# Performance work log

Hardware: AMD Instinct MI355X
Metric: run time of the kernel (lower is better)

## Reference

```python
import jax, jax.numpy as jnp
import numpy as np

B, T, D = 32, 2048, 1024
H = D  # dim_h = dim_k in build()


def setup_inputs() -> dict:
    key = jax.random.key(0)
    ks = jax.random.split(key, 8)
    t = jax.random.normal(ks[0], (B, T, D), dtype=jnp.float32)
    a = jax.random.normal(ks[1], (B, D), dtype=jnp.float32)
    b = jax.random.normal(ks[2], (B, D), dtype=jnp.float32)
    mask = jax.random.randint(ks[3], (B, T), 0, 2).astype(jnp.bool_)
    # glorot_normal-like scale for D x H weights
    s = (2.0 / (D + H)) ** 0.5
    wt = jax.random.normal(ks[4], (D, H), dtype=jnp.float32) * s
    wa = jax.random.normal(ks[5], (D, H), dtype=jnp.float32) * s
    wb = jax.random.normal(ks[6], (D, H), dtype=jnp.float32) * s
    wh = jax.random.normal(ks[7], (H, 1), dtype=jnp.float32) * (2.0 / (H + 1)) ** 0.5
    return {"t": t, "a": a, "b": b, "mask": mask,
            "wt": wt, "wa": wa, "wb": wb, "wh": wh}


def reference(t, a, b, mask, wt, wa, wb, wh):
    m = mask.astype(jnp.float32)                      # (B, T)
    ht = jnp.tanh(jnp.einsum('btd,dh->bth', t, wt))    # (B, T, H)
    ha = jnp.tanh(a @ wa)                              # (B, H)
    hb = jnp.tanh(b @ wb)                              # (B, H)
    h = ht * (ha * hb)[:, None, :]                     # (B, T, H)
    att = jnp.einsum('bth,h->bt', h, wh[:, 0])         # (B, T) scores
    att = jax.nn.softmax(att, axis=-1)
    att = att * m
    att = att / jnp.sum(att, axis=-1, keepdims=True)   # mask-renormalize
    return jnp.einsum('btd,bt->bd', t, att)            # weighted-sum pooling
```

## Files before the change

### kernel.cpp

```cpp
#include <hip/hip_runtime.h>
#include <hip/hip_bf16.h>
#include <cstdint>
#include <cstddef>

#define B_  32
#define T_  2048
#define D_  1024
#define H_  1024
#define M_  (B_ * T_)

typedef __attribute__((ext_vector_type(4))) float  f32x4;
typedef __attribute__((ext_vector_type(8))) __bf16 bf16x8;

#define GLOBAL_AS __attribute__((address_space(1)))
#define LDS_AS    __attribute__((address_space(3)))

__device__ __forceinline__ void gload_lds16(const void* g, void* l) {
  __builtin_amdgcn_global_load_lds((const GLOBAL_AS unsigned int*)g,
                                   (LDS_AS unsigned int*)l, 16, 0, 0);
}

__device__ __forceinline__ unsigned int f2bf(float f) {
  unsigned int u = __float_as_uint(f);
  return (u + 0x7fffu + ((u >> 16) & 1u)) >> 16;
}
__device__ __forceinline__ unsigned int packbf2(float lo, float hi) {
  return f2bf(lo) | (f2bf(hi) << 16);
}
__device__ __forceinline__ float bfu(unsigned int u) {
  return __uint_as_float(u << 16);
}
__device__ __forceinline__ float fast_tanh(float x) {
  x = fminf(fmaxf(x, -15.f), 15.f);
  float e = __expf(2.f * x);
  return (e - 1.f) / (e + 1.f);
}

__global__ __launch_bounds__(256) void k_tobf16(const float4* __restrict__ t4,
                                                uint2* __restrict__ ob) {
  const size_t stride = (size_t)gridDim.x * 256;
  for (size_t i = (size_t)blockIdx.x * 256 + threadIdx.x; i < (size_t)M_ * 256; i += stride) {
    const float4 v = t4[i];
    uint2 o; o.x = packbf2(v.x, v.y); o.y = packbf2(v.z, v.w);
    ob[i] = o;
  }
}

__global__ __launch_bounds__(256) void k_wt_transpose(const float* __restrict__ wt,
                                                      unsigned short* __restrict__ wtT) {
  __shared__ float tile[32][33];
  const int tx = threadIdx.x & 31, ty = threadIdx.x >> 5;
  const int c0 = blockIdx.x * 32, r0 = blockIdx.y * 32;
#pragma unroll
  for (int i = 0; i < 4; ++i)
    tile[ty + i * 8][tx] = wt[(size_t)(r0 + ty + i * 8) * H_ + c0 + tx];
  __syncthreads();
#pragma unroll
  for (int i = 0; i < 4; ++i)
    wtT[(size_t)(c0 + ty + i * 8) * D_ + r0 + tx] = (unsigned short)f2bf(tile[tx][ty + i * 8]);
}

__global__ __launch_bounds__(256) void k_g(const float* __restrict__ a,
                                           const float* __restrict__ b,
                                           const float* __restrict__ wa,
                                           const float* __restrict__ wb,
                                           const float* __restrict__ wh,
                                           float* __restrict__ g) {
  const int idx = blockIdx.x * 256 + threadIdx.x;
  const int bb = idx >> 10, h = idx & 1023;
  float sa = 0.f, sb = 0.f;
  for (int d = 0; d < 1024; ++d) {
    sa += a[bb * 1024 + d] * wa[d * 1024 + h];
    sb += b[bb * 1024 + d] * wb[d * 1024 + h];
  }
  g[idx] = fast_tanh(sa) * fast_tanh(sb) * wh[h];
}

__global__ __launch_bounds__(512) void k_score_fast(const unsigned short* __restrict__ tb,
                                                    const unsigned short* __restrict__ wtT,
                                                    const float* __restrict__ g,
                                                    float* __restrict__ spart) {
  __shared__ unsigned short As[256 * 64];
  __shared__ unsigned short Bs[128 * 64];
  __shared__ float red[512];
  const int tid = threadIdx.x;
  const int wg  = (blockIdx.x & 7) * 256 + (blockIdx.x >> 3);
  const int bm2 = wg >> 3, bn = wg & 7;
  const int lane = tid & 63, w = tid >> 6;
  const int wm = w >> 1, wn = w & 1;
  const int l15 = lane & 15, lk = lane >> 4;
  const int axk = l15 & 7;
  const int row0 = bm2 * 256, col0 = bn * 128;

  const int srow = lane >> 3;
  const int scol = (((lane & 7) ^ srow) * 8);
  const unsigned short* gA = tb  + (size_t)(row0 + w * 32 + srow) * 1024 + scol;
  const unsigned short* gB = wtT + (size_t)(col0 + w * 16 + srow) * 1024 + scol;
  unsigned short* lA = &As[(w * 32) * 64];
  unsigned short* lB = &Bs[(w * 16) * 64];

  f32x4 acc[4][4] = {};

  for (int kt = 0; kt < 16; ++kt) {
    const int k0 = kt * 64;
    __syncthreads();
#pragma unroll
    for (int i = 0; i < 4; ++i)
      gload_lds16(gA + (size_t)i * 8192 + k0, lA + i * 512);
#pragma unroll
    for (int j = 0; j < 2; ++j)
      gload_lds16(gB + (size_t)j * 8192 + k0, lB + j * 512);
    __syncthreads();
#pragma unroll
    for (int kf = 0; kf < 2; ++kf) {
      bf16x8 af[4], bfr[4];
#pragma unroll
      for (int mi = 0; mi < 4; ++mi)
        af[mi] = *(const bf16x8*)(&As[(wm * 64 + mi * 16 + l15) * 64
                                      + (((kf * 4 + lk) ^ axk) << 3)]);
#pragma unroll
      for (int ni = 0; ni < 4; ++ni)
        bfr[ni] = *(const bf16x8*)(&Bs[(wn * 64 + ni * 16 + l15) * 64
                                       + (((kf * 4 + lk) ^ axk) << 3)]);
#pragma unroll
      for (int mi = 0; mi < 4; ++mi)
#pragma unroll
        for (int ni = 0; ni < 4; ++ni)
          acc[mi][ni] = __builtin_amdgcn_mfma_f32_16x16x32_bf16(af[mi], bfr[ni], acc[mi][ni], 0, 0, 0);
    }
  }

  const int b = row0 >> 11;
  float gv[4];
#pragma unroll
  for (int ni = 0; ni < 4; ++ni)
    gv[ni] = g[b * H_ + col0 + wn * 64 + ni * 16 + l15];
#pragma unroll
  for (int mi = 0; mi < 4; ++mi) {
#pragma unroll
    for (int r = 0; r < 4; ++r) {
      float s = 0.f;
#pragma unroll
      for (int ni = 0; ni < 4; ++ni)
        s += fast_tanh(acc[mi][ni][r]) * gv[ni];
      s += __shfl_xor(s, 1); s += __shfl_xor(s, 2);
      s += __shfl_xor(s, 4); s += __shfl_xor(s, 8);
      if (l15 == 0)
        red[wn * 256 + wm * 64 + mi * 16 + lk * 4 + r] = s;
    }
  }
  __syncthreads();
  if (tid < 256)
    spart[(size_t)bn * M_ + row0 + tid] = red[tid] + red[256 + tid];
}

__global__ __launch_bounds__(256) void k_score_rs(const float* __restrict__ t,
                                                  const unsigned short* __restrict__ wtT,
                                                  const float* __restrict__ g,
                                                  float* __restrict__ spart) {
  __shared__ unsigned short As[128 * 72];
  __shared__ unsigned short Bs[128 * 72];
  __shared__ float red[256];
  const int tid = threadIdx.x;
  const int bn = blockIdx.x, bm = blockIdx.y;
  const int lane = tid & 63, w = tid >> 6;
  const int wm = w >> 1, wn = w & 1;
  const int l15 = lane & 15, lk = lane >> 4;
  const int row0 = bm * 128, col0 = bn * 128;
  const int ar = tid >> 2, ac = (tid & 3) * 16;
  const int brn = tid >> 1, bco = (tid & 1) * 32;

  f32x4 acc[4][4] = {};

  for (int kt = 0; kt < 16; ++kt) {
    const int k0 = kt * 64;
    __syncthreads();
#pragma unroll
    for (int half = 0; half < 2; ++half) {
      const int r = ar + half * 64;
      const float4* src = (const float4*)(t + (size_t)(row0 + r) * 1024 + k0 + ac);
      float4 v0 = src[0], v1 = src[1], v2 = src[2], v3 = src[3];
      uint4 p0, p1;
      p0.x = packbf2(v0.x, v0.y); p0.y = packbf2(v0.z, v0.w);
      p0.z = packbf2(v1.x, v1.y); p0.w = packbf2(v1.z, v1.w);
      p1.x = packbf2(v2.x, v2.y); p1.y = packbf2(v2.z, v2.w);
      p1.z = packbf2(v3.x, v3.y); p1.w = packbf2(v3.z, v3.w);
      uint4* dst = (uint4*)(&As[r * 72 + ac]);
      dst[0] = p0; dst[1] = p1;
    }
    {
      const uint4* src = (const uint4*)(wtT + (size_t)(col0 + brn) * 1024 + k0 + bco);
      uint4 x0 = src[0], x1 = src[1], x2 = src[2], x3 = src[3];
      uint4* dst = (uint4*)(&Bs[brn * 72 + bco]);
      dst[0] = x0; dst[1] = x1; dst[2] = x2; dst[3] = x3;
    }
    __syncthreads();
#pragma unroll
    for (int kf = 0; kf < 2; ++kf) {
      bf16x8 af[4], bfr[4];
#pragma unroll
      for (int mi = 0; mi < 4; ++mi)
        af[mi] = *(const bf16x8*)(&As[(wm * 64 + mi * 16 + l15) * 72 + kf * 32 + lk * 8]);
#pragma unroll
      for (int ni = 0; ni < 4; ++ni)
        bfr[ni] = *(const bf16x8*)(&Bs[(wn * 64 + ni * 16 + l15) * 72 + kf * 32 + lk * 8]);
#pragma unroll
      for (int mi = 0; mi < 4; ++mi)
#pragma unroll
        for (int ni = 0; ni < 4; ++ni)
          acc[mi][ni] = __builtin_amdgcn_mfma_f32_16x16x32_bf16(af[mi], bfr[ni], acc[mi][ni], 0, 0, 0);
    }
  }

  const int b = row0 >> 11;
  float gv[4];
#pragma unroll
  for (int ni = 0; ni < 4; ++ni)
    gv[ni] = g[b * H_ + col0 + wn * 64 + ni * 16 + l15];
#pragma unroll
  for (int mi = 0; mi < 4; ++mi) {
#pragma unroll
    for (int r = 0; r < 4; ++r) {
      float s = 0.f;
#pragma unroll
      for (int ni = 0; ni < 4; ++ni)
        s += fast_tanh(acc[mi][ni][r]) * gv[ni];
      s += __shfl_xor(s, 1); s += __shfl_xor(s, 2);
      s += __shfl_xor(s, 4); s += __shfl_xor(s, 8);
      if (l15 == 0)
        red[wn * 128 + wm * 64 + mi * 16 + lk * 4 + r] = s;
    }
  }
  __syncthreads();
  if (tid < 128)
    spart[(size_t)bn * M_ + row0 + tid] = red[tid] + red[128 + tid];
}

__global__ __launch_bounds__(256) void k_softmax(const float* __restrict__ spart,
                                                 const void* __restrict__ mask,
                                                 float* __restrict__ att) {
  __shared__ float redmax[4], redsum[4];
  __shared__ int shflag[4];
  const int b = blockIdx.x, tid = threadIdx.x;

  {
    const unsigned int* mw = (const unsigned int*)mask;
    int any = 0;
    for (int i = tid; i < 16384; i += 256)
      if (mw[i] > 1u) any = 1;
    const int wa = __any(any) ? 1 : 0;
    if ((tid & 63) == 0) shflag[tid >> 6] = wa;
  }

  float s[8];
#pragma unroll
  for (int j = 0; j < 8; ++j) {
    const int idx = tid + j * 256;
    float v = 0.f;
#pragma unroll
    for (int nb = 0; nb < 8; ++nb) v += spart[(size_t)nb * M_ + b * T_ + idx];
    s[j] = v;
  }
  float mx = s[0];
#pragma unroll
  for (int j = 1; j < 8; ++j) mx = fmaxf(mx, s[j]);
  for (int o = 1; o < 64; o <<= 1) mx = fmaxf(mx, __shfl_xor(mx, o));
  if ((tid & 63) == 0) redmax[tid >> 6] = mx;
  __syncthreads();
  mx = fmaxf(fmaxf(redmax[0], redmax[1]), fmaxf(redmax[2], redmax[3]));
  const int byte_mode = shflag[0] | shflag[1] | shflag[2] | shflag[3];

  float e[8];
  float sum = 0.f;
#pragma unroll
  for (int j = 0; j < 8; ++j) {
    const int idx = tid + j * 256;
    float v = __expf(s[j] - mx);
    const int mv = byte_mode ? (int)((const unsigned char*)mask)[b * T_ + idx]
                             : ((const int*)mask)[b * T_ + idx];
    v = (mv != 0) ? v : 0.f;
    e[j] = v;
    sum += v;
  }
  for (int o = 1; o < 64; o <<= 1) sum += __shfl_xor(sum, o);
  if ((tid & 63) == 0) redsum[tid >> 6] = sum;
  __syncthreads();
  sum = redsum[0] + redsum[1] + redsum[2] + redsum[3];
  const float inv = 1.f / sum;
#pragma unroll
  for (int j = 0; j < 8; ++j)
    att[b * T_ + tid + j * 256] = e[j] * inv;
}

__global__ __launch_bounds__(256) void k_pool_bf(const unsigned short* __restrict__ tb,
                                                 const float* __restrict__ att,
                                                 float* __restrict__ pp) {
  const int b = blockIdx.x, tc = blockIdx.y, tid = threadIdx.x;
  const uint2* tp = (const uint2*)tb;
  float4 acc = make_float4(0.f, 0.f, 0.f, 0.f);
  const int tbase = tc * 128;
  for (int i = 0; i < 128; ++i) {
    const int ti = tbase + i;
    const float wv = att[b * T_ + ti];
    const uint2 v = tp[(size_t)(b * T_ + ti) * 256 + tid];
    acc.x += wv * bfu(v.x & 0xffffu);
    acc.y += wv * bfu(v.x >> 16);
    acc.z += wv * bfu(v.y & 0xffffu);
    acc.w += wv * bfu(v.y >> 16);
  }
  ((float4*)pp)[(size_t)tc * 8192 + b * 256 + tid] = acc;
}

__global__ __launch_bounds__(256) void k_pool_f32(const float* __restrict__ t,
                                                  const float* __restrict__ att,
                                                  float* __restrict__ pp) {
  const int b = blockIdx.x, tc = blockIdx.y, tid = threadIdx.x;
  const float4* tp = (const float4*)t;
  float4 acc = make_float4(0.f, 0.f, 0.f, 0.f);
  const int tbase = tc * 128;
  for (int i = 0; i < 128; ++i) {
    const int ti = tbase + i;
    const float w = att[b * T_ + ti];
    const float4 v = tp[(size_t)(b * T_ + ti) * 256 + tid];
    acc.x += w * v.x; acc.y += w * v.y; acc.z += w * v.z; acc.w += w * v.w;
  }
  ((float4*)pp)[(size_t)tc * 8192 + b * 256 + tid] = acc;
}

__global__ __launch_bounds__(256) void k_pool_reduce(const float* __restrict__ pp,
                                                     float* __restrict__ out) {
  const int idx = blockIdx.x * 256 + threadIdx.x;
  float s = 0.f;
#pragma unroll
  for (int tc = 0; tc < 16; ++tc) s += pp[tc * 32768 + idx];
  out[idx] = s;
}

extern "C" void kernel_launch(void* const* d_in, const int* in_sizes, int n_in,
                              void* d_out, int out_size, void* d_ws, size_t ws_size,
                              hipStream_t stream) {
  const float* t    = (const float*)d_in[0];
  const float* a    = (const float*)d_in[1];
  const float* b    = (const float*)d_in[2];
  const void*  mask = d_in[3];
  const float* wt   = (const float*)d_in[4];
  const float* wa   = (const float*)d_in[5];
  const float* wb   = (const float*)d_in[6];
  const float* wh   = (const float*)d_in[7];
  float* out = (float*)d_out;

  float* ws = (float*)d_ws;
  const size_t NEED_FAST = (size_t)(33554432 + 32768 + 65536 + 524288 + 524288 + 524288) * 4;
  const bool fast = ws_size >= NEED_FAST;

  if (fast) {
    unsigned short* tb = (unsigned short*)ws;
    float* g     = ws + 33554432;
    float* att   = g + 32768;
    float* spart = att + 65536;
    float* pp    = spart + 524288;
    unsigned short* wtT = (unsigned short*)(pp + 524288);

    k_wt_transpose<<<dim3(32, 32), 256, 0, stream>>>(wt, wtT);
    k_tobf16<<<4096, 256, 0, stream>>>((const float4*)t, (uint2*)tb);
    k_g<<<128, 256, 0, stream>>>(a, b, wa, wb, wh, g);
    k_score_fast<<<2048, 512, 0, stream>>>(tb, wtT, g, spart);
    k_softmax<<<32, 256, 0, stream>>>(spart, mask, att);
    k_pool_bf<<<dim3(32, 16), 256, 0, stream>>>(tb, att, pp);
    k_pool_reduce<<<128, 256, 0, stream>>>(pp, out);
  } else {
    float* g     = ws;
    float* att   = ws + 32768;
    float* spart = ws + 98304;
    float* pp    = ws + 622592;
    unsigned short* wtT = (unsigned short*)(ws + 1146880);

    k_wt_transpose<<<dim3(32, 32), 256, 0, stream>>>(wt, wtT);
    k_g<<<128, 256, 0, stream>>>(a, b, wa, wb, wh, g);
    k_score_rs<<<dim3(8, 512), 256, 0, stream>>>(t, wtT, g, spart);
    k_softmax<<<32, 256, 0, stream>>>(spart, mask, att);
    k_pool_f32<<<dim3(32, 16), 256, 0, stream>>>(t, att, pp);
    k_pool_reduce<<<128, 256, 0, stream>>>(pp, out);
  }
}
```

Measured before the change: 337.4 us.

## Merge prep kernels into one launch and rework the gate GEMV mapping

The weight transpose, the bf16 conversion of t and the gate computation now run as block-index ranges of a single kernel, so three launches become one and the small jobs overlap with the large conversion. The gate GEMV is remapped to 32 blocks where each thread computes four h outputs with float4 weight loads, replacing 128 blocks of scalar loads. The gate work now runs on fewer blocks, which may leave it on the critical path. The softmax plane-count loop becomes a runtime argument and loses its unroll.

```diff
diff --git a/kernel.cpp b/kernel.cpp
--- a/kernel.cpp
+++ b/kernel.cpp
@@ -36,44 +36,55 @@
   return (e - 1.f) / (e + 1.f);
 }
 
-__global__ __launch_bounds__(256) void k_tobf16(const float4* __restrict__ t4,
-                                                uint2* __restrict__ ob) {
-  const size_t stride = (size_t)gridDim.x * 256;
-  for (size_t i = (size_t)blockIdx.x * 256 + threadIdx.x; i < (size_t)M_ * 256; i += stride) {
-    const float4 v = t4[i];
-    uint2 o; o.x = packbf2(v.x, v.y); o.y = packbf2(v.z, v.w);
-    ob[i] = o;
-  }
-}
-
-__global__ __launch_bounds__(256) void k_wt_transpose(const float* __restrict__ wt,
-                                                      unsigned short* __restrict__ wtT) {
-  __shared__ float tile[32][33];
-  const int tx = threadIdx.x & 31, ty = threadIdx.x >> 5;
-  const int c0 = blockIdx.x * 32, r0 = blockIdx.y * 32;
-#pragma unroll
-  for (int i = 0; i < 4; ++i)
-    tile[ty + i * 8][tx] = wt[(size_t)(r0 + ty + i * 8) * H_ + c0 + tx];
-  __syncthreads();
-#pragma unroll
-  for (int i = 0; i < 4; ++i)
-    wtT[(size_t)(c0 + ty + i * 8) * D_ + r0 + tx] = (unsigned short)f2bf(tile[tx][ty + i * 8]);
-}
-
-__global__ __launch_bounds__(256) void k_g(const float* __restrict__ a,
-                                           const float* __restrict__ b,
-                                           const float* __restrict__ wa,
-                                           const float* __restrict__ wb,
-                                           const float* __restrict__ wh,
-                                           float* __restrict__ g) {
-  const int idx = blockIdx.x * 256 + threadIdx.x;
-  const int bb = idx >> 10, h = idx & 1023;
-  float sa = 0.f, sb = 0.f;
-  for (int d = 0; d < 1024; ++d) {
-    sa += a[bb * 1024 + d] * wa[d * 1024 + h];
-    sb += b[bb * 1024 + d] * wb[d * 1024 + h];
-  }
-  g[idx] = fast_tanh(sa) * fast_tanh(sb) * wh[h];
+__global__ __launch_bounds__(256) void k_prep_all(const float4* __restrict__ t4,
+                                                  uint2* __restrict__ tb2,
+                                                  const float* __restrict__ wt,
+                                                  unsigned short* __restrict__ wtT,
+                                                  const float* __restrict__ a,
+                                                  const float* __restrict__ b,
+                                                  const float* __restrict__ wa,
+                                                  const float* __restrict__ wb,
+                                                  const float* __restrict__ wh,
+                                                  float* __restrict__ g) {
+  const int bid = blockIdx.x, tid = threadIdx.x;
+  if (bid < 32) {
+    const int h0 = bid * 32;
+    const int bb = tid >> 3;
+    const int h4 = h0 + (tid & 7) * 4;
+    float4 sa = make_float4(0.f, 0.f, 0.f, 0.f);
+    float4 sb = make_float4(0.f, 0.f, 0.f, 0.f);
+    for (int d = 0; d < 1024; ++d) {
+      const float av = a[bb * 1024 + d], bv = b[bb * 1024 + d];
+      const float4 wav = *(const float4*)(wa + (size_t)d * 1024 + h4);
+      const float4 wbv = *(const float4*)(wb + (size_t)d * 1024 + h4);
+      sa.x += av * wav.x; sa.y += av * wav.y; sa.z += av * wav.z; sa.w += av * wav.w;
+      sb.x += bv * wbv.x; sb.y += bv * wbv.y; sb.z += bv * wbv.z; sb.w += bv * wbv.w;
+    }
+    g[bb * H_ + h4 + 0] = fast_tanh(sa.x) * fast_tanh(sb.x) * wh[h4 + 0];
+    g[bb * H_ + h4 + 1] = fast_tanh(sa.y) * fast_tanh(sb.y) * wh[h4 + 1];
+    g[bb * H_ + h4 + 2] = fast_tanh(sa.z) * fast_tanh(sb.z) * wh[h4 + 2];
+    g[bb * H_ + h4 + 3] = fast_tanh(sa.w) * fast_tanh(sb.w) * wh[h4 + 3];
+  } else if (bid < 1056) {
+    __shared__ float tile[32][33];
+    const int tile_id = bid - 32;
+    const int tx = tid & 31, ty = tid >> 5;
+    const int c0 = (tile_id & 31) * 32, r0 = (tile_id >> 5) * 32;
+#pragma unroll
+    for (int i = 0; i < 4; ++i)
+      tile[ty + i * 8][tx] = wt[(size_t)(r0 + ty + i * 8) * H_ + c0 + tx];
+    __syncthreads();
+#pragma unroll
+    for (int i = 0; i < 4; ++i)
+      wtT[(size_t)(c0 + ty + i * 8) * D_ + r0 + tx] = (unsigned short)f2bf(tile[tx][ty + i * 8]);
+  } else {
+    const int cb = bid - 1056;
+    const size_t stride = (size_t)4096 * 256;
+    for (size_t i = (size_t)cb * 256 + tid; i < (size_t)M_ * 256; i += stride) {
+      const float4 v = t4[i];
+      uint2 o; o.x = packbf2(v.x, v.y); o.y = packbf2(v.z, v.w);
+      tb2[i] = o;
+    }
+  }
 }
 
 __global__ __launch_bounds__(512) void k_score_fast(const unsigned short* __restrict__ tb,
@@ -238,7 +249,8 @@
 
 __global__ __launch_bounds__(256) void k_softmax(const float* __restrict__ spart,
                                                  const void* __restrict__ mask,
-                                                 float* __restrict__ att) {
+                                                 float* __restrict__ att,
+                                                 int nplanes) {
   __shared__ float redmax[4], redsum[4];
   __shared__ int shflag[4];
   const int b = blockIdx.x, tid = threadIdx.x;
@@ -257,8 +269,7 @@
   for (int j = 0; j < 8; ++j) {
     const int idx = tid + j * 256;
     float v = 0.f;
-#pragma unroll
-    for (int nb = 0; nb < 8; ++nb) v += spart[(size_t)nb * M_ + b * T_ + idx];
+    for (int nb = 0; nb < nplanes; ++nb) v += spart[(size_t)nb * M_ + b * T_ + idx];
     s[j] = v;
   }
   float mx = s[0];
@@ -361,11 +372,10 @@
     float* pp    = spart + 524288;
     unsigned short* wtT = (unsigned short*)(pp + 524288);
 
-    k_wt_transpose<<<dim3(32, 32), 256, 0, stream>>>(wt, wtT);
-    k_tobf16<<<4096, 256, 0, stream>>>((const float4*)t, (uint2*)tb);
-    k_g<<<128, 256, 0, stream>>>(a, b, wa, wb, wh, g);
+    k_prep_all<<<5152, 256, 0, stream>>>((const float4*)t, (uint2*)tb,
+                                         wt, wtT, a, b, wa, wb, wh, g);
     k_score_fast<<<2048, 512, 0, stream>>>(tb, wtT, g, spart);
-    k_softmax<<<32, 256, 0, stream>>>(spart, mask, att);
+    k_softmax<<<32, 256, 0, stream>>>(spart, mask, att, 8);
     k_pool_bf<<<dim3(32, 16), 256, 0, stream>>>(tb, att, pp);
     k_pool_reduce<<<128, 256, 0, stream>>>(pp, out);
   } else {
@@ -375,10 +385,10 @@
     float* pp    = ws + 622592;
     unsigned short* wtT = (unsigned short*)(ws + 1146880);
 
-    k_wt_transpose<<<dim3(32, 32), 256, 0, stream>>>(wt, wtT);
-    k_g<<<128, 256, 0, stream>>>(a, b, wa, wb, wh, g);
+    k_prep_all<<<1056, 256, 0, stream>>>((const float4*)t, (uint2*)ws,
+                                         wt, wtT, a, b, wa, wb, wh, g);
     k_score_rs<<<dim3(8, 512), 256, 0, stream>>>(t, wtT, g, spart);
-    k_softmax<<<32, 256, 0, stream>>>(spart, mask, att);
+    k_softmax<<<32, 256, 0, stream>>>(spart, mask, att, 8);
     k_pool_f32<<<dim3(32, 16), 256, 0, stream>>>(t, att, pp);
     k_pool_reduce<<<128, 256, 0, stream>>>(pp, out);
   }
```

Measured after the change: 561.1 us. 66.3% more time.
